# Optimization experiments

Measured on AMD Instinct MI355X. Metric: run time of the kernel, lower is better.

Reference implementation:

```python
import jax, jax.numpy as jnp
import numpy as np

B, T, E = 2, 4096, 768
N_HEADS = 12
HEAD_DIM = E // N_HEADS


def setup_inputs() -> dict:
    key = jax.random.key(0)
    k1, k2, k3 = jax.random.split(key, 3)
    x = jax.random.normal(k1, (B, T, E), dtype=jnp.float32)
    W_attn = jax.random.normal(k2, (E, 3 * E), dtype=jnp.float32) * (1.0 / np.sqrt(E))
    b_attn = jnp.zeros((3 * E,), dtype=jnp.float32)
    W_proj = jax.random.normal(k3, (E, E), dtype=jnp.float32) * (1.0 / np.sqrt(E))
    b_proj = jnp.zeros((E,), dtype=jnp.float32)
    return {"x": x, "W_attn": W_attn, "b_attn": b_attn, "W_proj": W_proj, "b_proj": b_proj}


def reference(x, W_attn, b_attn, W_proj, b_proj):
    Bx, Tx, Ex = x.shape
    qkv = x @ W_attn + b_attn                      # [B,T,3E]
    q, k, v = jnp.split(qkv, 3, axis=-1)
    # [B,T,E] -> [B,H,T,D]
    def to_heads(t):
        return t.reshape(Bx, Tx, N_HEADS, HEAD_DIM).transpose(0, 2, 1, 3)
    q, k, v = to_heads(q), to_heads(k), to_heads(v)
    scale = 1.0 / np.sqrt(HEAD_DIM).astype(np.float32)
    scores = jnp.einsum('bhqd,bhkd->bhqk', q, k) * scale  # [B,H,T,T]
    causal = jnp.tril(jnp.ones((Tx, Tx), dtype=bool))
    scores = jnp.where(causal[None, None, :, :], scores, -jnp.inf)
    probs = jax.nn.softmax(scores, axis=-1)
    y = jnp.einsum('bhqk,bhkd->bhqd', probs, v)    # [B,H,T,D]
    y = y.transpose(0, 2, 1, 3).reshape(Bx, Tx, Ex)
    return y @ W_proj + b_proj
```

## Files before the change

### kernel.cpp

```cpp
#include <hip/hip_runtime.h>


#define SEQT 4096
#define EMB  768
#define NHEAD 12
#define HDIM 64

typedef __attribute__((ext_vector_type(8))) short bf16x8;
typedef __attribute__((ext_vector_type(4))) float f32x4;
typedef __attribute__((ext_vector_type(16))) float f32x16;

static __device__ __forceinline__ unsigned short f2bf(float f) {
  union { float f; unsigned u; } a; a.f = f;
  unsigned u = a.u;
  u += 0x7FFF + ((u >> 16) & 1);
  return (unsigned short)(u >> 16);
}

static __device__ __forceinline__ unsigned pack_bf16(float a, float b) {
  union { float f; unsigned u; } ua, ub; ua.f = a; ub.f = b;
  return __builtin_amdgcn_perm(ub.u + 0x8000u, ua.u + 0x8000u, 0x07060302u);
}

static __device__ __forceinline__ void gload_lds16(const short* g, short* l) {
  __builtin_amdgcn_global_load_lds(
      (const __attribute__((address_space(1))) unsigned*)(const void*)g,
      (__attribute__((address_space(3))) unsigned*)(void*)l, 16, 0, 0);
}

__global__ __launch_bounds__(256) void cast_bf16_kernel(
    const float* __restrict__ in, short* __restrict__ out, int n4) {
  int i = blockIdx.x * 256 + threadIdx.x;
  if (i >= n4) return;
  float4 v = ((const float4*)in)[i];
  ushort4 o;
  o.x = f2bf(v.x); o.y = f2bf(v.y); o.z = f2bf(v.z); o.w = f2bf(v.w);
  ((ushort4*)out)[i] = o;
}

__global__ __launch_bounds__(256) void transpose_bf16_kernel(
    const float* __restrict__ in, short* __restrict__ out, int R, int C) {
  __shared__ float tile[32][33];
  int c0 = blockIdx.x * 32, r0 = blockIdx.y * 32;
  int tx = threadIdx.x, ty = threadIdx.y;
#pragma unroll
  for (int j = 0; j < 32; j += 8)
    tile[ty + j][tx] = in[(size_t)(r0 + ty + j) * C + (c0 + tx)];
  __syncthreads();
#pragma unroll
  for (int j = 0; j < 32; j += 8)
    out[(size_t)(c0 + ty + j) * R + (r0 + tx)] = (short)f2bf(tile[tx][ty + j]);
}

template <int MODE>
__global__ __launch_bounds__(256) void gemm128_kernel(
    const short* __restrict__ A, const short* __restrict__ Bt,
    const float* __restrict__ bias, int K,
    short* __restrict__ Qg, short* __restrict__ Kg, short* __restrict__ Vtg,
    float* __restrict__ Out) {
  __shared__ short As[128 * 32];
  __shared__ short Bs[128 * 32];
  int tid = threadIdx.x;
  int w = tid >> 6, l = tid & 63, quad = l >> 4, lo = l & 15;
  int wm = (w >> 1) * 64, wn = (w & 1) * 64;
  int gm = blockIdx.x, gn = blockIdx.y;
  f32x4 acc[4][4] = {};
  int c0 = tid, c1 = tid + 256;
  const short* Ag0 = A + (size_t)(gm * 128 + (c0 >> 2)) * K + (c0 & 3) * 8;
  const short* Ag1 = A + (size_t)(gm * 128 + (c1 >> 2)) * K + (c1 & 3) * 8;
  const short* Bg0 = Bt + (size_t)(gn * 128 + (c0 >> 2)) * K + (c0 & 3) * 8;
  const short* Bg1 = Bt + (size_t)(gn * 128 + (c1 >> 2)) * K + (c1 & 3) * 8;

  for (int kk = 0; kk < K; kk += 32) {
    gload_lds16(Ag0 + kk, &As[c0 * 8]);
    gload_lds16(Ag1 + kk, &As[c1 * 8]);
    gload_lds16(Bg0 + kk, &Bs[c0 * 8]);
    gload_lds16(Bg1 + kk, &Bs[c1 * 8]);
    __syncthreads();
    bf16x8 af[4], bf[4];
#pragma unroll
    for (int mt = 0; mt < 4; mt++)
      af[mt] = *(const bf16x8*)&As[(wm + mt * 16 + lo) * 32 + quad * 8];
#pragma unroll
    for (int nt = 0; nt < 4; nt++)
      bf[nt] = *(const bf16x8*)&Bs[(wn + nt * 16 + lo) * 32 + quad * 8];
#pragma unroll
    for (int mt = 0; mt < 4; mt++)
#pragma unroll
      for (int nt = 0; nt < 4; nt++)
        acc[mt][nt] = __builtin_amdgcn_mfma_f32_16x16x32_bf16(af[mt], bf[nt], acc[mt][nt], 0, 0, 0);
    __syncthreads();
  }

#pragma unroll
  for (int nt = 0; nt < 4; nt++) {
    int n = gn * 128 + wn + nt * 16 + lo;
    float bias_v = bias[n];
#pragma unroll
    for (int mt = 0; mt < 4; mt++) {
#pragma unroll
      for (int r = 0; r < 4; r++) {
        int m = gm * 128 + wm + mt * 16 + quad * 4 + r;
        float v = acc[mt][nt][r] + bias_v;
        if (MODE == 0) {
          int b = m >> 12, t = m & 4095;
          if (n < EMB) {
            int h = n >> 6, d = n & 63;
            Qg[(((size_t)b * NHEAD + h) * SEQT + t) * HDIM + d] = (short)f2bf(v);
          } else if (n < 2 * EMB) {
            int n2 = n - EMB, h = n2 >> 6, d = n2 & 63;
            Kg[(((size_t)b * NHEAD + h) * SEQT + t) * HDIM + d] = (short)f2bf(v);
          } else {
            int n2 = n - 2 * EMB, h = n2 >> 6, d = n2 & 63;
            Vtg[(((size_t)b * NHEAD + h) * HDIM + d) * SEQT + t] = (short)f2bf(v);
          }
        } else {
          Out[(size_t)m * EMB + n] = v;
        }
      }
    }
  }
}

#define AP 72
#define NEG_BIG (-1e9f)
__global__ __launch_bounds__(256, 2) void attn_kernel(
    const short* __restrict__ Qg, const short* __restrict__ Kg,
    const short* __restrict__ Vtg, short* __restrict__ Y) {
  __shared__ short Ks[64 * AP];
  __shared__ short Vs[64 * AP];
  int tid = threadIdx.x;
  int w = tid >> 6, l = tid & 63;
  int li = l & 31, hi = l >> 5;
  int bid = blockIdx.x;
  int qt = 15 - bid / 24;
  int bh = bid % 24;
  int q0 = qt * 256;
  int b = bh / NHEAD, h = bh % NHEAD;
  const short* Qbase = Qg + (size_t)bh * SEQT * HDIM;
  const short* Kbase = Kg + (size_t)bh * SEQT * HDIM;
  const short* Vbase = Vtg + (size_t)bh * HDIM * SEQT;

  int qw = q0 + w * 64;
  bf16x8 qf[2][4];
#pragma unroll
  for (int s = 0; s < 2; s++)
#pragma unroll
    for (int kk = 0; kk < 4; kk++)
      qf[s][kk] = *(const bf16x8*)&Qbase[(size_t)(qw + s * 32 + li) * HDIM + kk * 16 + hi * 8];

  f32x16 O[2][2] = {};
  float m_s[2] = {NEG_BIG, NEG_BIG};
  float l_s[2] = {0.f, 0.f};

  int sr = tid >> 2, sc = tid & 3;
  const float SC = 0.18033688011112042f;
  int qe = qw + 64;
  int nkv = q0 + 256;

  for (int kv0 = 0; kv0 < nkv; kv0 += 64) {
    const short* kg = &Kbase[(size_t)(kv0 + sr) * HDIM + sc * 8];
    const short* vg = &Vbase[(size_t)sr * SEQT + kv0 + sc * 8];
    uint4 k0 = *(const uint4*)kg;
    uint4 k1 = *(const uint4*)(kg + 32);
    uint4 v0 = *(const uint4*)vg;
    uint4 v1 = *(const uint4*)(vg + 32);
    *(uint4*)&Ks[sr * AP + sc * 8] = k0;
    *(uint4*)&Ks[sr * AP + sc * 8 + 32] = k1;
    *(uint4*)&Vs[sr * AP + sc * 8] = v0;
    *(uint4*)&Vs[sr * AP + sc * 8 + 32] = v1;
    __syncthreads();

    if (kv0 < qe) {
      bf16x8 ka[2][4];
#pragma unroll
      for (int t = 0; t < 2; t++)
#pragma unroll
        for (int kk = 0; kk < 4; kk++)
          ka[t][kk] = *(const bf16x8*)&Ks[(t * 32 + li) * AP + kk * 16 + hi * 8];

      f32x16 st[2][2];
#pragma unroll
      for (int s = 0; s < 2; s++) {
        int qbs = qw + s * 32;
#pragma unroll
        for (int t = 0; t < 2; t++) {
          if (kv0 + t * 32 <= qbs + 31) {
            f32x16 a = {};
#pragma unroll
            for (int kk = 0; kk < 4; kk++)
              a = __builtin_amdgcn_mfma_f32_32x32x16_bf16(ka[t][kk], qf[s][kk], a, 0, 0, 0);
            st[s][t] = a;
          }
        }
      }

      bf16x8 va[2][4];
#pragma unroll
      for (int dt = 0; dt < 2; dt++)
#pragma unroll
        for (int g = 0; g < 4; g++)
          va[dt][g] = *(const bf16x8*)&Vs[(dt * 32 + li) * AP + g * 16 + hi * 8];

#pragma unroll
      for (int s = 0; s < 2; s++) {
        int qbs = qw + s * 32;
        if (kv0 > qbs + 31) continue;
        bool full0 = (kv0 + 31 <= qbs);
        bool act1 = (kv0 + 32 <= qbs + 31);
        bool full1 = (kv0 + 63 <= qbs);
        float mx = NEG_BIG;
        if (full0) {
#pragma unroll
          for (int r = 0; r < 16; r++) mx = fmaxf(mx, st[s][0][r]);
        } else {
          int thr = qbs - kv0 + li - 4 * hi;
#pragma unroll
          for (int r = 0; r < 16; r++) {
            const int R = (r & 3) + 8 * (r >> 2);
            st[s][0][r] = (R <= thr) ? st[s][0][r] : NEG_BIG;
            mx = fmaxf(mx, st[s][0][r]);
          }
        }
        if (act1) {
          if (full1) {
#pragma unroll
            for (int r = 0; r < 16; r++) mx = fmaxf(mx, st[s][1][r]);
          } else {
            int thr = qbs - kv0 - 32 + li - 4 * hi;
#pragma unroll
            for (int r = 0; r < 16; r++) {
              const int R = (r & 3) + 8 * (r >> 2);
              st[s][1][r] = (R <= thr) ? st[s][1][r] : NEG_BIG;
              mx = fmaxf(mx, st[s][1][r]);
            }
          }
        }
        mx = fmaxf(mx, __shfl_xor(mx, 32));
        float mn = fmaxf(m_s[s], mx);
        float c1 = SC * mn;
        float al = __builtin_amdgcn_exp2f(fminf(SC * m_s[s] - c1, 0.f));
        m_s[s] = mn;
        float sm = 0.f;
        unsigned pk[2][8];
#pragma unroll
        for (int r2 = 0; r2 < 8; r2++) {
          float pa = __builtin_amdgcn_exp2f(fminf(__builtin_fmaf(st[s][0][2 * r2],     SC, -c1), 0.f));
          float pb = __builtin_amdgcn_exp2f(fminf(__builtin_fmaf(st[s][0][2 * r2 + 1], SC, -c1), 0.f));
          sm += pa + pb;
          pk[0][r2] = pack_bf16(pa, pb);
        }
        if (act1) {
#pragma unroll
          for (int r2 = 0; r2 < 8; r2++) {
            float pa = __builtin_amdgcn_exp2f(fminf(__builtin_fmaf(st[s][1][2 * r2],     SC, -c1), 0.f));
            float pb = __builtin_amdgcn_exp2f(fminf(__builtin_fmaf(st[s][1][2 * r2 + 1], SC, -c1), 0.f));
            sm += pa + pb;
            pk[1][r2] = pack_bf16(pa, pb);
          }
        }
        sm += __shfl_xor(sm, 32);
        l_s[s] = l_s[s] * al + sm;
#pragma unroll
        for (int dt = 0; dt < 2; dt++)
#pragma unroll
          for (int r = 0; r < 16; r++) O[s][dt][r] *= al;

#pragma unroll
        for (int g = 0; g < 4; g++) {
          int t = g >> 1, k2 = g & 1;
          if (t == 1 && !act1) continue;
          unsigned own_a = hi ? pk[t][k2 * 4 + 2] : pk[t][k2 * 4 + 0];
          unsigned own_b = hi ? pk[t][k2 * 4 + 3] : pk[t][k2 * 4 + 1];
          unsigned snd_a = hi ? pk[t][k2 * 4 + 0] : pk[t][k2 * 4 + 2];
          unsigned snd_b = hi ? pk[t][k2 * 4 + 1] : pk[t][k2 * 4 + 3];
          unsigned rcv_a = (unsigned)__shfl_xor((int)snd_a, 32);
          unsigned rcv_b = (unsigned)__shfl_xor((int)snd_b, 32);
          union { unsigned u[4]; bf16x8 v; } pf;
          pf.u[0] = hi ? rcv_a : own_a;
          pf.u[1] = hi ? rcv_b : own_b;
          pf.u[2] = hi ? own_a : rcv_a;
          pf.u[3] = hi ? own_b : rcv_b;
#pragma unroll
          for (int dt = 0; dt < 2; dt++)
            O[s][dt] = __builtin_amdgcn_mfma_f32_32x32x16_bf16(va[dt][g], pf.v, O[s][dt], 0, 0, 0);
        }
      }
    }
    __syncthreads();
  }

#pragma unroll
  for (int s = 0; s < 2; s++) {
    float rl = 1.f / l_s[s];
    int q = qw + s * 32 + li;
    short* yp = &Y[((size_t)b * SEQT + q) * EMB + h * 64];
#pragma unroll
    for (int dt = 0; dt < 2; dt++) {
#pragma unroll
      for (int rg = 0; rg < 4; rg++) {
        uint2 u2;
        u2.x = pack_bf16(O[s][dt][rg * 4 + 0] * rl, O[s][dt][rg * 4 + 1] * rl);
        u2.y = pack_bf16(O[s][dt][rg * 4 + 2] * rl, O[s][dt][rg * 4 + 3] * rl);
        *(uint2*)(yp + dt * 32 + rg * 8 + hi * 4) = u2;
      }
    }
  }
}

extern "C" void kernel_launch(void* const* d_in, const int* in_sizes, int n_in,
                              void* d_out, int out_size, void* d_ws, size_t ws_size,
                              hipStream_t stream) {
  const float* x      = (const float*)d_in[0];
  const float* W_attn = (const float*)d_in[1];
  const float* b_attn = (const float*)d_in[2];
  const float* W_proj = (const float*)d_in[3];
  const float* b_proj = (const float*)d_in[4];
  float* out = (float*)d_out;

  char* ws = (char*)d_ws;
  short* x_bf = (short*)(ws + 0);
  short* Wt_a = (short*)(ws + 12582912);
  short* Wt_p = (short*)(ws + 16121856);
  short* Qg   = (short*)(ws + 17301504);
  short* Kg   = (short*)(ws + 29884416);
  short* Vtg  = (short*)(ws + 42467328);
  short* Ybf  = (short*)(ws + 55050240);

  cast_bf16_kernel<<<6144, 256, 0, stream>>>(x, x_bf, 1572864);
  transpose_bf16_kernel<<<dim3(72, 24), dim3(32, 8), 0, stream>>>(W_attn, Wt_a, 768, 2304);
  transpose_bf16_kernel<<<dim3(24, 24), dim3(32, 8), 0, stream>>>(W_proj, Wt_p, 768, 768);

  gemm128_kernel<0><<<dim3(64, 18), 256, 0, stream>>>(x_bf, Wt_a, b_attn, 768,
                                                      Qg, Kg, Vtg, nullptr);
  attn_kernel<<<384, 256, 0, stream>>>(Qg, Kg, Vtg, Ybf);
  gemm128_kernel<1><<<dim3(64, 6), 256, 0, stream>>>(Ybf, Wt_p, b_proj, 768,
                                                     nullptr, nullptr, nullptr, out);
}
```

Baseline: 334.4 us.

## Halve attention query tile, prefetch next KV tile into registers, vectorize QKV epilogue

The attention kernel now gives each block 128 queries instead of 256, with one 32-row slice per wave. This doubles the grid to 768 blocks and raises the occupancy hint to 3 blocks per CU, aiming at better load balance across CUs under the causal mask. The K/V tile for the next iteration is loaded into registers while the current one is being computed, overlapping global latency with compute. The QKV GEMM swaps its MFMA operands so each lane holds 4 consecutive output columns, which lets Q and K be written as packed 8-byte stores with a float4 bias load. In exchange, each K/V tile is loaded from global memory by twice as many blocks, and register pressure rises from the prefetch.

```diff
diff --git a/kernel.cpp b/kernel.cpp
--- a/kernel.cpp
+++ b/kernel.cpp
@@ -87,35 +87,57 @@
 #pragma unroll
     for (int mt = 0; mt < 4; mt++)
 #pragma unroll
-      for (int nt = 0; nt < 4; nt++)
-        acc[mt][nt] = __builtin_amdgcn_mfma_f32_16x16x32_bf16(af[mt], bf[nt], acc[mt][nt], 0, 0, 0);
+      for (int nt = 0; nt < 4; nt++) {
+        if (MODE == 0)
+          acc[mt][nt] = __builtin_amdgcn_mfma_f32_16x16x32_bf16(bf[nt], af[mt], acc[mt][nt], 0, 0, 0);
+        else
+          acc[mt][nt] = __builtin_amdgcn_mfma_f32_16x16x32_bf16(af[mt], bf[nt], acc[mt][nt], 0, 0, 0);
+      }
     __syncthreads();
   }
 
-#pragma unroll
-  for (int nt = 0; nt < 4; nt++) {
-    int n = gn * 128 + wn + nt * 16 + lo;
-    float bias_v = bias[n];
-#pragma unroll
-    for (int mt = 0; mt < 4; mt++) {
-#pragma unroll
-      for (int r = 0; r < 4; r++) {
-        int m = gm * 128 + wm + mt * 16 + quad * 4 + r;
-        float v = acc[mt][nt][r] + bias_v;
-        if (MODE == 0) {
-          int b = m >> 12, t = m & 4095;
-          if (n < EMB) {
-            int h = n >> 6, d = n & 63;
-            Qg[(((size_t)b * NHEAD + h) * SEQT + t) * HDIM + d] = (short)f2bf(v);
-          } else if (n < 2 * EMB) {
-            int n2 = n - EMB, h = n2 >> 6, d = n2 & 63;
-            Kg[(((size_t)b * NHEAD + h) * SEQT + t) * HDIM + d] = (short)f2bf(v);
-          } else {
-            int n2 = n - 2 * EMB, h = n2 >> 6, d = n2 & 63;
-            Vtg[(((size_t)b * NHEAD + h) * HDIM + d) * SEQT + t] = (short)f2bf(v);
-          }
+  if (MODE == 0) {
+#pragma unroll
+    for (int nt = 0; nt < 4; nt++) {
+      int nb = gn * 128 + wn + nt * 16 + quad * 4;
+      float4 bv = *(const float4*)&bias[nb];
+#pragma unroll
+      for (int mt = 0; mt < 4; mt++) {
+        int m = gm * 128 + wm + mt * 16 + lo;
+        int b = m >> 12, t = m & 4095;
+        float v0 = acc[mt][nt][0] + bv.x;
+        float v1 = acc[mt][nt][1] + bv.y;
+        float v2 = acc[mt][nt][2] + bv.z;
+        float v3 = acc[mt][nt][3] + bv.w;
+        if (nb < EMB) {
+          int h = nb >> 6, d = nb & 63;
+          uint2 u; u.x = pack_bf16(v0, v1); u.y = pack_bf16(v2, v3);
+          *(uint2*)&Qg[(((size_t)b * NHEAD + h) * SEQT + t) * HDIM + d] = u;
+        } else if (nb < 2 * EMB) {
+          int n2 = nb - EMB, h = n2 >> 6, d = n2 & 63;
+          uint2 u; u.x = pack_bf16(v0, v1); u.y = pack_bf16(v2, v3);
+          *(uint2*)&Kg[(((size_t)b * NHEAD + h) * SEQT + t) * HDIM + d] = u;
         } else {
-          Out[(size_t)m * EMB + n] = v;
+          int n2 = nb - 2 * EMB, h = n2 >> 6, d = n2 & 63;
+          short* vp = &Vtg[(((size_t)b * NHEAD + h) * HDIM + d) * SEQT + t];
+          vp[0] = (short)f2bf(v0);
+          vp[SEQT] = (short)f2bf(v1);
+          vp[2 * SEQT] = (short)f2bf(v2);
+          vp[3 * SEQT] = (short)f2bf(v3);
+        }
+      }
+    }
+  } else {
+#pragma unroll
+    for (int nt = 0; nt < 4; nt++) {
+      int n = gn * 128 + wn + nt * 16 + lo;
+      float bias_v = bias[n];
+#pragma unroll
+      for (int mt = 0; mt < 4; mt++) {
+#pragma unroll
+        for (int r = 0; r < 4; r++) {
+          int m = gm * 128 + wm + mt * 16 + quad * 4 + r;
+          Out[(size_t)m * EMB + n] = acc[mt][nt][r] + bias_v;
         }
       }
     }
@@ -124,7 +146,7 @@
 
 #define AP 72
 #define NEG_BIG (-1e9f)
-__global__ __launch_bounds__(256, 2) void attn_kernel(
+__global__ __launch_bounds__(256, 3) void attn_kernel(
     const short* __restrict__ Qg, const short* __restrict__ Kg,
     const short* __restrict__ Vtg, short* __restrict__ Y) {
   __shared__ short Ks[64 * AP];
@@ -133,66 +155,76 @@
   int w = tid >> 6, l = tid & 63;
   int li = l & 31, hi = l >> 5;
   int bid = blockIdx.x;
-  int qt = 15 - bid / 24;
+  int qt = 31 - bid / 24;
   int bh = bid % 24;
-  int q0 = qt * 256;
+  int q0 = qt * 128;
   int b = bh / NHEAD, h = bh % NHEAD;
   const short* Qbase = Qg + (size_t)bh * SEQT * HDIM;
   const short* Kbase = Kg + (size_t)bh * SEQT * HDIM;
   const short* Vbase = Vtg + (size_t)bh * HDIM * SEQT;
 
-  int qw = q0 + w * 64;
-  bf16x8 qf[2][4];
-#pragma unroll
-  for (int s = 0; s < 2; s++)
-#pragma unroll
-    for (int kk = 0; kk < 4; kk++)
-      qf[s][kk] = *(const bf16x8*)&Qbase[(size_t)(qw + s * 32 + li) * HDIM + kk * 16 + hi * 8];
-
-  f32x16 O[2][2] = {};
-  float m_s[2] = {NEG_BIG, NEG_BIG};
-  float l_s[2] = {0.f, 0.f};
+  int qw = q0 + w * 32;
+  bf16x8 qf[4];
+#pragma unroll
+  for (int kk = 0; kk < 4; kk++)
+    qf[kk] = *(const bf16x8*)&Qbase[(size_t)(qw + li) * HDIM + kk * 16 + hi * 8];
+
+  f32x16 O[2] = {};
+  float m_s = NEG_BIG;
+  float l_s = 0.f;
 
   int sr = tid >> 2, sc = tid & 3;
   const float SC = 0.18033688011112042f;
-  int qe = qw + 64;
-  int nkv = q0 + 256;
+  int nkv = q0 + 128;
+
+  uint4 ck0, ck1, cv0, cv1;
+  {
+    const short* kg = &Kbase[(size_t)sr * HDIM + sc * 8];
+    const short* vg = &Vbase[(size_t)sr * SEQT + sc * 8];
+    ck0 = *(const uint4*)kg;  ck1 = *(const uint4*)(kg + 32);
+    cv0 = *(const uint4*)vg;  cv1 = *(const uint4*)(vg + 32);
+  }
 
   for (int kv0 = 0; kv0 < nkv; kv0 += 64) {
-    const short* kg = &Kbase[(size_t)(kv0 + sr) * HDIM + sc * 8];
-    const short* vg = &Vbase[(size_t)sr * SEQT + kv0 + sc * 8];
-    uint4 k0 = *(const uint4*)kg;
-    uint4 k1 = *(const uint4*)(kg + 32);
-    uint4 v0 = *(const uint4*)vg;
-    uint4 v1 = *(const uint4*)(vg + 32);
-    *(uint4*)&Ks[sr * AP + sc * 8] = k0;
-    *(uint4*)&Ks[sr * AP + sc * 8 + 32] = k1;
-    *(uint4*)&Vs[sr * AP + sc * 8] = v0;
-    *(uint4*)&Vs[sr * AP + sc * 8 + 32] = v1;
+    *(uint4*)&Ks[sr * AP + sc * 8] = ck0;
+    *(uint4*)&Ks[sr * AP + sc * 8 + 32] = ck1;
+    *(uint4*)&Vs[sr * AP + sc * 8] = cv0;
+    *(uint4*)&Vs[sr * AP + sc * 8 + 32] = cv1;
     __syncthreads();
 
-    if (kv0 < qe) {
-      bf16x8 ka[2][4];
-#pragma unroll
-      for (int t = 0; t < 2; t++)
+    if (kv0 + 64 < nkv) {
+      const short* kg = &Kbase[(size_t)(kv0 + 64 + sr) * HDIM + sc * 8];
+      const short* vg = &Vbase[(size_t)sr * SEQT + kv0 + 64 + sc * 8];
+      ck0 = *(const uint4*)kg;  ck1 = *(const uint4*)(kg + 32);
+      cv0 = *(const uint4*)vg;  cv1 = *(const uint4*)(vg + 32);
+    }
+
+    if (kv0 <= qw) {
+      bool act1 = (kv0 + 32 <= qw);
+      bf16x8 ka0[4], ka1[4];
+#pragma unroll
+      for (int kk = 0; kk < 4; kk++)
+        ka0[kk] = *(const bf16x8*)&Ks[li * AP + kk * 16 + hi * 8];
+      if (act1) {
 #pragma unroll
         for (int kk = 0; kk < 4; kk++)
-          ka[t][kk] = *(const bf16x8*)&Ks[(t * 32 + li) * AP + kk * 16 + hi * 8];
-
-      f32x16 st[2][2];
-#pragma unroll
-      for (int s = 0; s < 2; s++) {
-        int qbs = qw + s * 32;
-#pragma unroll
-        for (int t = 0; t < 2; t++) {
-          if (kv0 + t * 32 <= qbs + 31) {
-            f32x16 a = {};
-#pragma unroll
-            for (int kk = 0; kk < 4; kk++)
-              a = __builtin_amdgcn_mfma_f32_32x32x16_bf16(ka[t][kk], qf[s][kk], a, 0, 0, 0);
-            st[s][t] = a;
-          }
-        }
+          ka1[kk] = *(const bf16x8*)&Ks[(32 + li) * AP + kk * 16 + hi * 8];
+      }
+
+      f32x16 st[2];
+      {
+        f32x16 a = {};
+#pragma unroll
+        for (int kk = 0; kk < 4; kk++)
+          a = __builtin_amdgcn_mfma_f32_32x32x16_bf16(ka0[kk], qf[kk], a, 0, 0, 0);
+        st[0] = a;
+      }
+      if (act1) {
+        f32x16 a = {};
+#pragma unroll
+        for (int kk = 0; kk < 4; kk++)
+          a = __builtin_amdgcn_mfma_f32_32x32x16_bf16(ka1[kk], qf[kk], a, 0, 0, 0);
+        st[1] = a;
       }
 
       bf16x8 va[2][4];
@@ -202,108 +234,99 @@
         for (int g = 0; g < 4; g++)
           va[dt][g] = *(const bf16x8*)&Vs[(dt * 32 + li) * AP + g * 16 + hi * 8];
 
-#pragma unroll
-      for (int s = 0; s < 2; s++) {
-        int qbs = qw + s * 32;
-        if (kv0 > qbs + 31) continue;
-        bool full0 = (kv0 + 31 <= qbs);
-        bool act1 = (kv0 + 32 <= qbs + 31);
-        bool full1 = (kv0 + 63 <= qbs);
-        float mx = NEG_BIG;
-        if (full0) {
-#pragma unroll
-          for (int r = 0; r < 16; r++) mx = fmaxf(mx, st[s][0][r]);
+      bool full0 = (kv0 < qw);
+      float mx = NEG_BIG;
+      if (full0) {
+#pragma unroll
+        for (int r = 0; r < 16; r++) mx = fmaxf(mx, st[0][r]);
+      } else {
+        int thr = li - 4 * hi;
+#pragma unroll
+        for (int r = 0; r < 16; r++) {
+          const int R = (r & 3) + 8 * (r >> 2);
+          st[0][r] = (R <= thr) ? st[0][r] : NEG_BIG;
+          mx = fmaxf(mx, st[0][r]);
+        }
+      }
+      if (act1) {
+        bool full1 = (kv0 + 32 < qw);
+        if (full1) {
+#pragma unroll
+          for (int r = 0; r < 16; r++) mx = fmaxf(mx, st[1][r]);
         } else {
-          int thr = qbs - kv0 + li - 4 * hi;
+          int thr = li - 4 * hi;
 #pragma unroll
           for (int r = 0; r < 16; r++) {
             const int R = (r & 3) + 8 * (r >> 2);
-            st[s][0][r] = (R <= thr) ? st[s][0][r] : NEG_BIG;
-            mx = fmaxf(mx, st[s][0][r]);
+            st[1][r] = (R <= thr) ? st[1][r] : NEG_BIG;
+            mx = fmaxf(mx, st[1][r]);
           }
         }
-        if (act1) {
-          if (full1) {
-#pragma unroll
-            for (int r = 0; r < 16; r++) mx = fmaxf(mx, st[s][1][r]);
-          } else {
-            int thr = qbs - kv0 - 32 + li - 4 * hi;
-#pragma unroll
-            for (int r = 0; r < 16; r++) {
-              const int R = (r & 3) + 8 * (r >> 2);
-              st[s][1][r] = (R <= thr) ? st[s][1][r] : NEG_BIG;
-              mx = fmaxf(mx, st[s][1][r]);
-            }
-          }
-        }
-        mx = fmaxf(mx, __shfl_xor(mx, 32));
-        float mn = fmaxf(m_s[s], mx);
-        float c1 = SC * mn;
-        float al = __builtin_amdgcn_exp2f(fminf(SC * m_s[s] - c1, 0.f));
-        m_s[s] = mn;
-        float sm = 0.f;
-        unsigned pk[2][8];
+      }
+      mx = fmaxf(mx, __shfl_xor(mx, 32));
+      float mn = fmaxf(m_s, mx);
+      float c1 = SC * mn;
+      float al = __builtin_amdgcn_exp2f(fminf(SC * m_s - c1, 0.f));
+      m_s = mn;
+      float sm = 0.f;
+      unsigned pk[2][8];
+#pragma unroll
+      for (int r2 = 0; r2 < 8; r2++) {
+        float pa = __builtin_amdgcn_exp2f(fminf(__builtin_fmaf(st[0][2 * r2],     SC, -c1), 0.f));
+        float pb = __builtin_amdgcn_exp2f(fminf(__builtin_fmaf(st[0][2 * r2 + 1], SC, -c1), 0.f));
+        sm += pa + pb;
+        pk[0][r2] = pack_bf16(pa, pb);
+      }
+      if (act1) {
 #pragma unroll
         for (int r2 = 0; r2 < 8; r2++) {
-          float pa = __builtin_amdgcn_exp2f(fminf(__builtin_fmaf(st[s][0][2 * r2],     SC, -c1), 0.f));
-          float pb = __builtin_amdgcn_exp2f(fminf(__builtin_fmaf(st[s][0][2 * r2 + 1], SC, -c1), 0.f));
+          float pa = __builtin_amdgcn_exp2f(fminf(__builtin_fmaf(st[1][2 * r2],     SC, -c1), 0.f));
+          float pb = __builtin_amdgcn_exp2f(fminf(__builtin_fmaf(st[1][2 * r2 + 1], SC, -c1), 0.f));
           sm += pa + pb;
-          pk[0][r2] = pack_bf16(pa, pb);
-        }
-        if (act1) {
-#pragma unroll
-          for (int r2 = 0; r2 < 8; r2++) {
-            float pa = __builtin_amdgcn_exp2f(fminf(__builtin_fmaf(st[s][1][2 * r2],     SC, -c1), 0.f));
-            float pb = __builtin_amdgcn_exp2f(fminf(__builtin_fmaf(st[s][1][2 * r2 + 1], SC, -c1), 0.f));
-            sm += pa + pb;
-            pk[1][r2] = pack_bf16(pa, pb);
-          }
-        }
-        sm += __shfl_xor(sm, 32);
-        l_s[s] = l_s[s] * al + sm;
+          pk[1][r2] = pack_bf16(pa, pb);
+        }
+      }
+      sm += __shfl_xor(sm, 32);
+      l_s = l_s * al + sm;
+#pragma unroll
+      for (int dt = 0; dt < 2; dt++)
+#pragma unroll
+        for (int r = 0; r < 16; r++) O[dt][r] *= al;
+
+#pragma unroll
+      for (int g = 0; g < 4; g++) {
+        int t = g >> 1, k2 = g & 1;
+        if (t == 1 && !act1) continue;
+        unsigned own_a = hi ? pk[t][k2 * 4 + 2] : pk[t][k2 * 4 + 0];
+        unsigned own_b = hi ? pk[t][k2 * 4 + 3] : pk[t][k2 * 4 + 1];
+        unsigned snd_a = hi ? pk[t][k2 * 4 + 0] : pk[t][k2 * 4 + 2];
+        unsigned snd_b = hi ? pk[t][k2 * 4 + 1] : pk[t][k2 * 4 + 3];
+        unsigned rcv_a = (unsigned)__shfl_xor((int)snd_a, 32);
+        unsigned rcv_b = (unsigned)__shfl_xor((int)snd_b, 32);
+        union { unsigned u[4]; bf16x8 v; } pf;
+        pf.u[0] = hi ? rcv_a : own_a;
+        pf.u[1] = hi ? rcv_b : own_b;
+        pf.u[2] = hi ? own_a : rcv_a;
+        pf.u[3] = hi ? own_b : rcv_b;
 #pragma unroll
         for (int dt = 0; dt < 2; dt++)
-#pragma unroll
-          for (int r = 0; r < 16; r++) O[s][dt][r] *= al;
-
-#pragma unroll
-        for (int g = 0; g < 4; g++) {
-          int t = g >> 1, k2 = g & 1;
-          if (t == 1 && !act1) continue;
-          unsigned own_a = hi ? pk[t][k2 * 4 + 2] : pk[t][k2 * 4 + 0];
-          unsigned own_b = hi ? pk[t][k2 * 4 + 3] : pk[t][k2 * 4 + 1];
-          unsigned snd_a = hi ? pk[t][k2 * 4 + 0] : pk[t][k2 * 4 + 2];
-          unsigned snd_b = hi ? pk[t][k2 * 4 + 1] : pk[t][k2 * 4 + 3];
-          unsigned rcv_a = (unsigned)__shfl_xor((int)snd_a, 32);
-          unsigned rcv_b = (unsigned)__shfl_xor((int)snd_b, 32);
-          union { unsigned u[4]; bf16x8 v; } pf;
-          pf.u[0] = hi ? rcv_a : own_a;
-          pf.u[1] = hi ? rcv_b : own_b;
-          pf.u[2] = hi ? own_a : rcv_a;
-          pf.u[3] = hi ? own_b : rcv_b;
-#pragma unroll
-          for (int dt = 0; dt < 2; dt++)
-            O[s][dt] = __builtin_amdgcn_mfma_f32_32x32x16_bf16(va[dt][g], pf.v, O[s][dt], 0, 0, 0);
-        }
+          O[dt] = __builtin_amdgcn_mfma_f32_32x32x16_bf16(va[dt][g], pf.v, O[dt], 0, 0, 0);
       }
     }
     __syncthreads();
   }
 
-#pragma unroll
-  for (int s = 0; s < 2; s++) {
-    float rl = 1.f / l_s[s];
-    int q = qw + s * 32 + li;
-    short* yp = &Y[((size_t)b * SEQT + q) * EMB + h * 64];
-#pragma unroll
-    for (int dt = 0; dt < 2; dt++) {
-#pragma unroll
-      for (int rg = 0; rg < 4; rg++) {
-        uint2 u2;
-        u2.x = pack_bf16(O[s][dt][rg * 4 + 0] * rl, O[s][dt][rg * 4 + 1] * rl);
-        u2.y = pack_bf16(O[s][dt][rg * 4 + 2] * rl, O[s][dt][rg * 4 + 3] * rl);
-        *(uint2*)(yp + dt * 32 + rg * 8 + hi * 4) = u2;
-      }
+  float rl = 1.f / l_s;
+  int q = qw + li;
+  short* yp = &Y[((size_t)b * SEQT + q) * EMB + h * 64];
+#pragma unroll
+  for (int dt = 0; dt < 2; dt++) {
+#pragma unroll
+    for (int rg = 0; rg < 4; rg++) {
+      uint2 u2;
+      u2.x = pack_bf16(O[dt][rg * 4 + 0] * rl, O[dt][rg * 4 + 1] * rl);
+      u2.y = pack_bf16(O[dt][rg * 4 + 2] * rl, O[dt][rg * 4 + 3] * rl);
+      *(uint2*)(yp + dt * 32 + rg * 8 + hi * 4) = u2;
     }
   }
 }
@@ -333,7 +356,7 @@
 
   gemm128_kernel<0><<<dim3(64, 18), 256, 0, stream>>>(x_bf, Wt_a, b_attn, 768,
                                                       Qg, Kg, Vtg, nullptr);
-  attn_kernel<<<384, 256, 0, stream>>>(Qg, Kg, Vtg, Ybf);
+  attn_kernel<<<768, 256, 0, stream>>>(Qg, Kg, Vtg, Ybf);
   gemm128_kernel<1><<<dim3(64, 6), 256, 0, stream>>>(Ybf, Wt_p, b_proj, 768,
                                                      nullptr, nullptr, nullptr, out);
 }
```

Result: faster. 310.6 us (-7.1%).
